# Kernel tuning notes

Measured on AMD Instinct MI355X. Metric: run time of the kernel, lower is better.

## Reference

```python
import jax, jax.numpy as jnp
import numpy as np

B = 2048
IN_FEATURES = 512
OUT_FEATURES = 32768
S = 64.0   # arcface default scale
M = 0.5    # arcface default margin
EPS = 1e-7


def _l2_normalize(x, axis=-1):
    # matches torch F.normalize(p=2, eps=1e-12)
    n = jnp.sqrt(jnp.sum(x * x, axis=axis, keepdims=True))
    return x / jnp.maximum(n, 1e-12)


def setup_inputs() -> dict:
    key = jax.random.key(0)
    k1, k2, k3 = jax.random.split(key, 3)
    features = jax.random.normal(k1, (B, IN_FEATURES), dtype=jnp.float32)
    y_true = jax.random.randint(k2, (B,), 0, OUT_FEATURES)
    # xavier_uniform_ for weight of shape (out, in)
    limit = float(np.sqrt(6.0 / (OUT_FEATURES + IN_FEATURES)))
    weight = jax.random.uniform(k3, (OUT_FEATURES, IN_FEATURES), dtype=jnp.float32,
                                minval=-limit, maxval=limit)
    return {"features": features, "y_true": y_true, "weight": weight}


def reference(features, y_true, weight):
    f = _l2_normalize(features)            # [B, D]
    w = _l2_normalize(weight)              # [C, D]
    wf = jnp.einsum('bd,cd->bc', f, w)     # [B, C] cosine logits
    tgt = wf[jnp.arange(wf.shape[0]), y_true]  # [B]
    # arcface margin transform
    numerator = S * jnp.cos(jnp.arccos(jnp.clip(tgt, -1.0 + EPS, 1.0 - EPS)) + M)
    # sum of exp(s*wf) over all non-target classes = full sum minus target term
    excl_sum = jnp.sum(jnp.exp(S * wf), axis=1) - jnp.exp(S * tgt)
    denominator = jnp.exp(numerator) + excl_sum
    L = numerator - jnp.log(denominator)
    return -jnp.mean(L)
```

## Files before the change

kernel.cpp:

```cpp
#include <hip/hip_runtime.h>
#include <hip/hip_bf16.h>
#include <math.h>


#define BN 2048
#define DK 512
#define CN 32768

typedef __attribute__((ext_vector_type(4))) float floatx4;

__device__ inline float dot4(floatx4 a, floatx4 b) {
  return a.x * b.x + a.y * b.y + a.z * b.z + a.w * b.w;
}

__device__ inline int pack_fp8x4(floatx4 v) {
  int r = __builtin_amdgcn_cvt_pk_fp8_f32(v.x, v.y, 0, false);
  r = __builtin_amdgcn_cvt_pk_fp8_f32(v.z, v.w, r, true);
  return r;
}

__device__ inline void async_ld16(const void* g, void* l) {
  __builtin_amdgcn_global_load_lds(
      (const __attribute__((address_space(1))) void*)g,
      (__attribute__((address_space(3))) void*)l, 16, 0, 0);
}

__global__ void prep_kernel(const float* __restrict__ feat,
                            const int* __restrict__ y,
                            const float* __restrict__ w,
                            int* __restrict__ fb8,
                            int* __restrict__ wb8,
                            float* __restrict__ tgt,
                            float* __restrict__ rowsum) {
  const int wave = threadIdx.x >> 6;
  const int l = threadIdx.x & 63;
  if (blockIdx.x < 8192) {
    const int row = blockIdx.x * 4 + wave;
    const floatx4* src = (const floatx4*)(w + (size_t)row * DK);
    floatx4 v0 = src[l];
    floatx4 v1 = src[64 + l];
    float s = dot4(v0, v0) + dot4(v1, v1);
#pragma unroll
    for (int off = 1; off < 64; off <<= 1) s += __shfl_xor(s, off, 64);
    const float scale = 1.0f / fmaxf(sqrtf(s), 1e-12f);
    v0 *= scale; v1 *= scale;
    int* db = wb8 + (size_t)row * 128;
    db[l] = pack_fp8x4(v0);
    db[64 + l] = pack_fp8x4(v1);
  } else {
    const int i = (blockIdx.x - 8192) * 4 + wave;
    const floatx4* src = (const floatx4*)(feat + (size_t)i * DK);
    floatx4 v0 = src[l];
    floatx4 v1 = src[64 + l];
    const int cls = y[i];
    const floatx4* wr = (const floatx4*)(w + (size_t)cls * DK);
    floatx4 w0 = wr[l], w1 = wr[64 + l];
    float s  = dot4(v0, v0) + dot4(v1, v1);
    float d  = dot4(v0, w0) + dot4(v1, w1);
    float wn = dot4(w0, w0) + dot4(w1, w1);
#pragma unroll
    for (int off = 1; off < 64; off <<= 1) {
      s  += __shfl_xor(s, off, 64);
      d  += __shfl_xor(d, off, 64);
      wn += __shfl_xor(wn, off, 64);
    }
    const float fscale = 1.0f / fmaxf(sqrtf(s), 1e-12f);
    v0 *= fscale; v1 *= fscale;
    int* db = fb8 + (size_t)i * 128;
    db[l] = pack_fp8x4(v0);
    db[64 + l] = pack_fp8x4(v1);
    if (l == 0) {
      tgt[i] = d * fscale / fmaxf(sqrtf(wn), 1e-12f);
      rowsum[i] = 0.0f;
    }
  }
}

__launch_bounds__(512, 4)
__global__ void gemm_exp_kernel(const char* __restrict__ fb8,
                                const char* __restrict__ wb8,
                                float* __restrict__ rowsum) {
  __shared__ char As[128 * 64];
  __shared__ char Bs[256 * 64];
  __shared__ float lsum[128];

  const int tid  = threadIdx.x;
  const int wave = tid >> 6;
  const int lane = tid & 63;

  const int n = blockIdx.x;
  const int tileM = ((n >> 3) & 15) * 128;
  const int tileN = (((n >> 7) << 3) | (n & 7)) * 256;

  const int wm = (wave >> 2) * 64;
  const int wn = (wave & 3) * 64;

  if (tid < 128) lsum[tid] = 0.0f;

  floatx4 acc[4][4];
#pragma unroll
  for (int mi = 0; mi < 4; ++mi)
#pragma unroll
    for (int ni = 0; ni < 4; ++ni)
      acc[mi][ni] = (floatx4){0.f, 0.f, 0.f, 0.f};

  const int mA = tid >> 2;
  const int uA = (tid & 3) ^ ((mA >> 1) & 3);
  const int mB0 = tid >> 2;
  const int uB0 = (tid & 3) ^ ((mB0 >> 1) & 3);
  const int mB1 = (512 + tid) >> 2;
  const int uB1 = (tid & 3) ^ ((mB1 >> 1) & 3);
  const char* gA  = fb8 + (size_t)(tileM + mA)  * DK + uA  * 16;
  const char* gB0 = wb8 + (size_t)(tileN + mB0) * DK + uB0 * 16;
  const char* gB1 = wb8 + (size_t)(tileN + mB1) * DK + uB1 * 16;
  char* lA  = &As[wave * 1024];
  char* lB0 = &Bs[wave * 1024];
  char* lB1 = &Bs[8192 + wave * 1024];

  const int mrow = lane & 15;
  const int q    = lane >> 4;
  const int qh   = q >> 1;
  const int qb   = (q & 1) * 8;

  for (int kk = 0; kk < DK / 64; ++kk) {
    __syncthreads();
    async_ld16(gA,  lA);
    async_ld16(gB0, lB0);
    async_ld16(gB1, lB1);
    gA += 64; gB0 += 64; gB1 += 64;
    __syncthreads();

#pragma unroll
    for (int p = 0; p < 2; ++p) {
      long af[4], bf[4];
#pragma unroll
      for (int mi = 0; mi < 4; ++mi) {
        const int row = wm + mi * 16 + mrow;
        const int st = (2 * p + qh) ^ ((row >> 1) & 3);
        af[mi] = *(const long*)&As[row * 64 + st * 16 + qb];
      }
#pragma unroll
      for (int ni = 0; ni < 4; ++ni) {
        const int row = wn + ni * 16 + mrow;
        const int st = (2 * p + qh) ^ ((row >> 1) & 3);
        bf[ni] = *(const long*)&Bs[row * 64 + st * 16 + qb];
      }
#pragma unroll
      for (int mi = 0; mi < 4; ++mi)
#pragma unroll
        for (int ni = 0; ni < 4; ++ni)
          acc[mi][ni] = __builtin_amdgcn_mfma_f32_16x16x32_fp8_fp8(
              af[mi], bf[ni], acc[mi][ni], 0, 0, 0);
    }
  }

  const int rowq = (lane >> 4) * 4;
#pragma unroll
  for (int mi = 0; mi < 4; ++mi) {
#pragma unroll
    for (int r = 0; r < 4; ++r) {
      float v = 0.f;
#pragma unroll
      for (int ni = 0; ni < 4; ++ni)
        v += __expf(64.0f * acc[mi][ni][r]);
      v += __shfl_xor(v, 1, 64);
      v += __shfl_xor(v, 2, 64);
      v += __shfl_xor(v, 4, 64);
      v += __shfl_xor(v, 8, 64);
      if ((lane & 15) == 0)
        atomicAdd(&lsum[wm + mi * 16 + rowq + r], v);
    }
  }
  __syncthreads();
  if (tid < 128)
    atomicAdd(&rowsum[tileM + tid], lsum[tid]);
}

__global__ void loss_kernel(const float* __restrict__ tgt,
                            const float* __restrict__ rowsum,
                            float* __restrict__ out) {
  __shared__ float wsum[8];
  const int t = threadIdx.x;
  float sum = 0.f;
  const float cM = 0.87758256189037271f;
  const float sM = 0.47942553860420301f;
  for (int i = t; i < BN; i += 512) {
    const float tg_raw = tgt[i];
    const float tg = fminf(fmaxf(tg_raw, -1.f + 1e-7f), 1.f - 1e-7f);
    const float num = 64.f * (tg * cM - sqrtf(fmaxf(1.f - tg * tg, 0.f)) * sM);
    const float den = expf(num) + rowsum[i] - expf(64.f * tg_raw);
    sum += num - logf(den);
  }
#pragma unroll
  for (int off = 1; off < 64; off <<= 1) sum += __shfl_xor(sum, off, 64);
  if ((t & 63) == 0) wsum[t >> 6] = sum;
  __syncthreads();
  if (t == 0) {
    float tot = 0.f;
#pragma unroll
    for (int k = 0; k < 8; ++k) tot += wsum[k];
    out[0] = -tot * (1.0f / (float)BN);
  }
}

extern "C" void kernel_launch(void* const* d_in, const int* in_sizes, int n_in,
                              void* d_out, int out_size, void* d_ws, size_t ws_size,
                              hipStream_t stream) {
  const float* features = (const float*)d_in[0];
  const int*   y_true   = (const int*)d_in[1];
  const float* weight   = (const float*)d_in[2];
  float* out = (float*)d_out;

  char* ws = (char*)d_ws;
  char* wb8    = ws;
  char* fb8    = ws + 16777216;
  float* tgt    = (float*)(ws + 17825792);
  float* rowsum = (float*)(ws + 17833984);

  prep_kernel<<<8192 + 512, 256, 0, stream>>>(features, y_true, weight,
                                              (int*)fb8, (int*)wb8, tgt, rowsum);
  gemm_exp_kernel<<<2048, 512, 0, stream>>>(fb8, wb8, rowsum);
  loss_kernel<<<1, 512, 0, stream>>>(tgt, rowsum, out);
}
```

Baseline: 161.3 us.

## Permute fp8 K-order in prep so GEMM reads fragments with 16-byte LDS loads

The prep kernel now writes the normalized fp8 rows in a permuted K order, so that each lane's two 8-byte MFMA fragments for the two k-substeps sit next to each other in memory. The GEMM loop then issues one 16-byte LDS read per row fragment instead of two 8-byte reads, halving the number of LDS load instructions. This is valid because the dot product does not depend on K ordering as long as features and weights share the same permutation. The swizzle pattern and bank-conflict behaviour change, and it relies on both operands being permuted the same way.

```diff
diff --git a/kernel.cpp b/kernel.cpp
--- a/kernel.cpp
+++ b/kernel.cpp
@@ -8,6 +8,7 @@
 #define CN 32768
 
 typedef __attribute__((ext_vector_type(4))) float floatx4;
+typedef __attribute__((ext_vector_type(2))) long longx2;
 
 __device__ inline float dot4(floatx4 a, floatx4 b) {
   return a.x * b.x + a.y * b.y + a.z * b.z + a.w * b.w;
@@ -17,6 +18,10 @@
   int r = __builtin_amdgcn_cvt_pk_fp8_f32(v.x, v.y, 0, false);
   r = __builtin_amdgcn_cvt_pk_fp8_f32(v.z, v.w, r, true);
   return r;
+}
+
+__device__ inline int permute16(int j) {
+  return ((j >> 1) & 3) * 4 + (j >> 3) * 2 + (j & 1);
 }
 
 __device__ inline void async_ld16(const void* g, void* l) {
@@ -34,6 +39,8 @@
                             float* __restrict__ rowsum) {
   const int wave = threadIdx.x >> 6;
   const int l = threadIdx.x & 63;
+  const int d0 = ((l >> 4) * 16)     + permute16(l & 15);
+  const int d1 = ((4 + (l >> 4)) * 16) + permute16(l & 15);
   if (blockIdx.x < 8192) {
     const int row = blockIdx.x * 4 + wave;
     const floatx4* src = (const floatx4*)(w + (size_t)row * DK);
@@ -45,8 +52,8 @@
     const float scale = 1.0f / fmaxf(sqrtf(s), 1e-12f);
     v0 *= scale; v1 *= scale;
     int* db = wb8 + (size_t)row * 128;
-    db[l] = pack_fp8x4(v0);
-    db[64 + l] = pack_fp8x4(v1);
+    db[d0] = pack_fp8x4(v0);
+    db[d1] = pack_fp8x4(v1);
   } else {
     const int i = (blockIdx.x - 8192) * 4 + wave;
     const floatx4* src = (const floatx4*)(feat + (size_t)i * DK);
@@ -67,8 +74,8 @@
     const float fscale = 1.0f / fmaxf(sqrtf(s), 1e-12f);
     v0 *= fscale; v1 *= fscale;
     int* db = fb8 + (size_t)i * 128;
-    db[l] = pack_fp8x4(v0);
-    db[64 + l] = pack_fp8x4(v1);
+    db[d0] = pack_fp8x4(v0);
+    db[d1] = pack_fp8x4(v1);
     if (l == 0) {
       tgt[i] = d * fscale / fmaxf(sqrtf(wn), 1e-12f);
       rowsum[i] = 0.0f;
@@ -119,8 +126,6 @@
 
   const int mrow = lane & 15;
   const int q    = lane >> 4;
-  const int qh   = q >> 1;
-  const int qb   = (q & 1) * 8;
 
   for (int kk = 0; kk < DK / 64; ++kk) {
     __syncthreads();
@@ -130,28 +135,33 @@
     gA += 64; gB0 += 64; gB1 += 64;
     __syncthreads();
 
-#pragma unroll
-    for (int p = 0; p < 2; ++p) {
-      long af[4], bf[4];
-#pragma unroll
-      for (int mi = 0; mi < 4; ++mi) {
-        const int row = wm + mi * 16 + mrow;
-        const int st = (2 * p + qh) ^ ((row >> 1) & 3);
-        af[mi] = *(const long*)&As[row * 64 + st * 16 + qb];
-      }
-#pragma unroll
-      for (int ni = 0; ni < 4; ++ni) {
-        const int row = wn + ni * 16 + mrow;
-        const int st = (2 * p + qh) ^ ((row >> 1) & 3);
-        bf[ni] = *(const long*)&Bs[row * 64 + st * 16 + qb];
-      }
-#pragma unroll
-      for (int mi = 0; mi < 4; ++mi)
-#pragma unroll
-        for (int ni = 0; ni < 4; ++ni)
-          acc[mi][ni] = __builtin_amdgcn_mfma_f32_16x16x32_fp8_fp8(
-              af[mi], bf[ni], acc[mi][ni], 0, 0, 0);
-    }
+    long af0[4], af1[4], bf0[4], bf1[4];
+#pragma unroll
+    for (int mi = 0; mi < 4; ++mi) {
+      const int row = wm + mi * 16 + mrow;
+      const int st = q ^ ((row >> 1) & 3);
+      longx2 t = *(const longx2*)&As[row * 64 + st * 16];
+      af0[mi] = t.x; af1[mi] = t.y;
+    }
+#pragma unroll
+    for (int ni = 0; ni < 4; ++ni) {
+      const int row = wn + ni * 16 + mrow;
+      const int st = q ^ ((row >> 1) & 3);
+      longx2 t = *(const longx2*)&Bs[row * 64 + st * 16];
+      bf0[ni] = t.x; bf1[ni] = t.y;
+    }
+#pragma unroll
+    for (int mi = 0; mi < 4; ++mi)
+#pragma unroll
+      for (int ni = 0; ni < 4; ++ni)
+        acc[mi][ni] = __builtin_amdgcn_mfma_f32_16x16x32_fp8_fp8(
+            af0[mi], bf0[ni], acc[mi][ni], 0, 0, 0);
+#pragma unroll
+    for (int mi = 0; mi < 4; ++mi)
+#pragma unroll
+      for (int ni = 0; ni < 4; ++ni)
+        acc[mi][ni] = __builtin_amdgcn_mfma_f32_16x16x32_fp8_fp8(
+            af1[mi], bf1[ni], acc[mi][ni], 0, 0, 0);
   }
 
   const int rowq = (lane >> 4) * 4;
```

Result: no change. 158.6 us (-1.7%).
